# Performance work log

Hardware: AMD Instinct MI355X
Metric: run time of the kernel (lower is better)

Reference implementation:

```python
import math
import jax, jax.numpy as jnp
import numpy as np

B, T, C, H = 1, 512, 768, 12
D = C // H           # head_dim = 64
TOPK_GATE = 128      # config.hoa_top_k
EPS = 1e-5


def _ln(x, w, b):
    m = x.mean(-1, keepdims=True)
    v = ((x - m) ** 2).mean(-1, keepdims=True)
    return (x - m) * jax.lax.rsqrt(v + EPS) * w + b


def _split_heads(x):  # (B,T,C) -> (B,H,T,D)
    return x.reshape(B, T, H, D).transpose(0, 2, 1, 3)


def _sdpa_causal(q, k, v):  # (B,H,T,D) each
    s = jnp.einsum('bhtd,bhsd->bhts', q, k) / math.sqrt(D)
    t = jnp.arange(T)
    s = jnp.where(t[:, None] >= t[None, :], s, -jnp.inf)
    return jnp.einsum('bhts,bhsd->bhtd', jax.nn.softmax(s, axis=-1), v)


def _gather_time(t4, idx):
    # t4: (B,H,T,D), idx: (B,H,T,k) -> (B,H,T,k,D)
    k = idx.shape[-1]
    src = jnp.broadcast_to(t4[:, :, :, None, :], (B, H, T, k, D))
    ind = jnp.broadcast_to(idx[..., None], (B, H, T, k, D))
    return jnp.take_along_axis(src, ind, axis=2)


def _hoa(x, wq, wk1, wk2, wv1, wv2, wo):
    # order-3 higher-order attention with per-branch top-k gathered keys/values
    k_keep = max(1, math.ceil(T ** (2.0 / 3.0)))  # 64 for T=512
    scale = D ** -0.5
    q = _split_heads(x @ wq)
    tar = jnp.arange(T)
    causal_ok = tar[:, None] >= tar[None, :]          # allowed positions
    j = jnp.arange(k_keep)
    # torch code pads short rows (t+1 < k_keep) by repeating the last valid topk idx
    clip = jnp.minimum(j[None, :], tar[:, None])      # (T, k_keep)
    gK, gV = [], []
    for wk, wv in ((wk1, wv1), (wk2, wv2)):
        K = _split_heads(x @ wk)
        V = _split_heads(x @ wv)
        logits = jnp.einsum('bhtd,bhsd->bhts', q, K) * scale
        logits = jnp.where(causal_ok[None, None], logits, -jnp.inf)
        idx = jax.lax.top_k(logits, k_keep)[1]        # (B,H,T,k_keep)
        idx = jnp.take_along_axis(idx, jnp.broadcast_to(clip, idx.shape), axis=-1)
        gK.append(_gather_time(K, idx))
        gV.append(_gather_time(V, idx))
    A = jnp.einsum('bhid,bhijd,bhikd->bhijk', q, gK[0], gK[1]) * scale
    alpha = jax.nn.softmax(A, axis=-1)                # softmax over LAST axis only (as torch)
    out = jnp.einsum('bhijk,bhijd,bhikd->bhid', alpha, gV[0], gV[1])
    return out.transpose(0, 2, 1, 3).reshape(B, T, C) @ wo


def _forward(x, ln1_w, ln1_b, qkv_w, qkv_b, atto_w, atto_b,
             lnh_w, lnh_b, hq_w, hk1_w, hk2_w, hv1_w, hv2_w, ho_w,
             gate_w, gate_b, ln2_w, ln2_b, fc_w, fc_b, pr_w, pr_b):
    # causal self-attention branch
    h = _ln(x, ln1_w, ln1_b)
    qkv = h @ qkv_w + qkv_b
    q, k, v = jnp.split(qkv, 3, axis=-1)
    y = _sdpa_causal(_split_heads(q), _split_heads(k), _split_heads(v))
    y = y.transpose(0, 2, 1, 3).reshape(B, T, C) @ atto_w + atto_b
    x = x + y
    # higher-order attention branch with gated top-k token mask
    hoa_in = _ln(x, lnh_w, lnh_b)
    hoa_out = _hoa(hoa_in, hq_w, hk1_w, hk2_w, hv1_w, hv2_w, ho_w)
    scores = (hoa_in @ gate_w + gate_b)[..., 0]       # (B,T)
    kk = min(TOPK_GATE, T)
    idx = jax.lax.top_k(scores, kk)[1]                # (B,kk)
    mask = jnp.zeros((B, T), x.dtype).at[jnp.arange(B)[:, None], idx].set(1.0)
    x = x + hoa_out * mask[..., None]
    # MLP
    h2 = _ln(x, ln2_w, ln2_b)
    x = x + (jax.nn.gelu(h2 @ fc_w + fc_b, approximate=False) @ pr_w + pr_b)
    return x


def setup_inputs() -> dict:
    key = jax.random.key(0)
    ks = jax.random.split(key, 13)
    def w(k, shape):
        return jax.random.normal(k, shape, jnp.float32) * 0.02
    return dict(
        x=jax.random.normal(ks[0], (B, T, C), jnp.float32),
        ln1_w=jnp.ones(C, jnp.float32), ln1_b=jnp.zeros(C, jnp.float32),
        qkv_w=w(ks[1], (C, 3 * C)), qkv_b=jnp.zeros(3 * C, jnp.float32),
        atto_w=w(ks[2], (C, C)), atto_b=jnp.zeros(C, jnp.float32),
        lnh_w=jnp.ones(C, jnp.float32), lnh_b=jnp.zeros(C, jnp.float32),
        hq_w=w(ks[3], (C, C)), hk1_w=w(ks[4], (C, C)), hk2_w=w(ks[5], (C, C)),
        hv1_w=w(ks[6], (C, C)), hv2_w=w(ks[7], (C, C)), ho_w=w(ks[8], (C, C)),
        gate_w=w(ks[9], (C, 1)), gate_b=jnp.zeros(1, jnp.float32),
        ln2_w=jnp.ones(C, jnp.float32), ln2_b=jnp.zeros(C, jnp.float32),
        fc_w=w(ks[10], (C, 4 * C)), fc_b=jnp.zeros(4 * C, jnp.float32),
        pr_w=w(ks[11], (4 * C, C)), pr_b=jnp.zeros(C, jnp.float32),
    )


def reference(x, ln1_w, ln1_b, qkv_w, qkv_b, atto_w, atto_b,
              lnh_w, lnh_b, hq_w, hk1_w, hk2_w, hv1_w, hv2_w, ho_w,
              gate_w, gate_b, ln2_w, ln2_b, fc_w, fc_b, pr_w, pr_b):
    return _forward(x, ln1_w, ln1_b, qkv_w, qkv_b, atto_w, atto_b,
                    lnh_w, lnh_b, hq_w, hk1_w, hk2_w, hv1_w, hv2_w, ho_w,
                    gate_w, gate_b, ln2_w, ln2_b, fc_w, fc_b, pr_w, pr_b)
```

## Files before the change

### kernel.cpp

```cpp
#include <hip/hip_runtime.h>
#include <hip/hip_bf16.h>
#include <math.h>

#define TT 512
#define CC 768
#define HH 12
#define DD 64
#define KKEEP 64
#define TOPG 128
#define NTCE (TT * CC)
#define NPAIR 36
#define PW (5 * CC)

typedef __attribute__((ext_vector_type(8))) short bf16x8;
typedef __attribute__((ext_vector_type(8))) unsigned short ushort8v;
typedef __attribute__((ext_vector_type(4))) float f32x4;
typedef unsigned long long u64;

__device__ __forceinline__ float block_sum(float v, float* red) {
#pragma unroll
  for (int off = 32; off; off >>= 1) v += __shfl_xor(v, off);
  __syncthreads();
  if ((threadIdx.x & 63) == 0) red[threadIdx.x >> 6] = v;
  __syncthreads();
  return red[0] + red[1] + red[2] + red[3];
}

__device__ __forceinline__ unsigned short f32_to_bf16_rne(float f) {
  unsigned u = __float_as_uint(f);
  unsigned r = (u + 0x7FFFu + ((u >> 16) & 1u)) >> 16;
  return (unsigned short)r;
}
__device__ __forceinline__ float bf16_to_f32(unsigned short h) {
  return __uint_as_float(((unsigned)h) << 16);
}
__device__ __forceinline__ void split2(float x, unsigned short& h, unsigned short& l) {
  h = f32_to_bf16_rne(x);
  l = f32_to_bf16_rne(x - bf16_to_f32(h));
}
__device__ __forceinline__ int swz(int row, int k) {
  return row * 64 + ((((k >> 3) ^ (row & 7))) << 3) + (k & 7);
}

struct WSplitArgs {
  const float* src[10];
  unsigned short* hi[10];
  unsigned short* lo[10];
  int K[10], N[10], tstart[10];
};

__global__ __launch_bounds__(256) void wsplitT_kernel(WSplitArgs a) {
  __shared__ float tile_[64][65];
  int t = blockIdx.x;
  int wsel = 0;
#pragma unroll
  for (int i = 1; i < 10; i++)
    if (t >= a.tstart[i]) wsel = i;
  int local = t - a.tstart[wsel];
  int K = a.K[wsel], N = a.N[wsel];
  int ntn = N >> 6;
  int bn = local % ntn, bk = local / ntn;
  int tid = threadIdx.x, r = tid >> 2, cq = tid & 3;
  const float* src = a.src[wsel] + (size_t)(bk * 64 + r) * N + bn * 64 + cq * 16;
#pragma unroll
  for (int f = 0; f < 4; f++) {
    float4 v = *(const float4*)(src + f * 4);
    tile_[r][cq * 16 + f * 4 + 0] = v.x;
    tile_[r][cq * 16 + f * 4 + 1] = v.y;
    tile_[r][cq * 16 + f * 4 + 2] = v.z;
    tile_[r][cq * 16 + f * 4 + 3] = v.w;
  }
  __syncthreads();
  size_t dst = (size_t)(bn * 64 + r) * K + bk * 64 + cq * 16;
  unsigned short hv[16], lv[16];
#pragma unroll
  for (int i = 0; i < 16; i++) split2(tile_[cq * 16 + i][r], hv[i], lv[i]);
  *(ushort8v*)&a.hi[wsel][dst] = *(const ushort8v*)&hv[0];
  *(ushort8v*)&a.hi[wsel][dst + 8] = *(const ushort8v*)&hv[8];
  *(ushort8v*)&a.lo[wsel][dst] = *(const ushort8v*)&lv[0];
  *(ushort8v*)&a.lo[wsel][dst + 8] = *(const ushort8v*)&lv[8];
}

__global__ void ln_bf_kernel(const float* __restrict__ x, const float* __restrict__ w,
                             const float* __restrict__ b,
                             unsigned short* __restrict__ ohi, unsigned short* __restrict__ olo,
                             const float* __restrict__ gw, const float* __restrict__ gb,
                             float* __restrict__ gscore) {
  int t = blockIdx.x, tid = threadIdx.x;
  __shared__ float red[4];
  float ls = 0.f;
  for (int c = tid; c < CC; c += 256) ls += x[t * CC + c];
  float mean = block_sum(ls, red) * (1.f / CC);
  float lv = 0.f;
  for (int c = tid; c < CC; c += 256) { float d = x[t * CC + c] - mean; lv += d * d; }
  float var = block_sum(lv, red) * (1.f / CC);
  float rs = rsqrtf(var + 1e-5f);
  float gpart = 0.f;
  for (int c = tid; c < CC; c += 256) {
    float val = (x[t * CC + c] - mean) * rs * w[c] + b[c];
    if (gscore) gpart += val * gw[c];
    unsigned short hb, lb;
    split2(val, hb, lb);
    ohi[t * CC + c] = hb;
    olo[t * CC + c] = lb;
  }
  if (gscore) {
    float s = block_sum(gpart, red);
    if (tid == 0) gscore[t] = s + gb[0];
  }
}

__global__ __launch_bounds__(256) void gemm_bf(
    const unsigned short* __restrict__ Ah, const unsigned short* __restrict__ Al,
    const unsigned short* __restrict__ Bh, const unsigned short* __restrict__ Bl,
    const float* __restrict__ bias, float* __restrict__ Cf,
    unsigned short* __restrict__ Chi, unsigned short* __restrict__ Clo,
    int M, int N, int K, int act, int seg, const float* __restrict__ res,
    const float* __restrict__ rowmask, float* __restrict__ part) {
  __shared__ unsigned short AsH[64 * 64], AsL[64 * 64], BsH[64 * 64], BsL[64 * 64];
  int tid = threadIdx.x, lane = tid & 63, wave = tid >> 6;
  int wr = wave >> 1, wc = wave & 1, lr = lane & 15;
  int ksub = (lane >> 4) * 8;
  int n0 = blockIdx.x * 64, m0 = blockIdx.y * 64;
  int lrow = tid >> 2, lq = tid & 3;
  int kchunk = K / gridDim.z;
  int kstart = blockIdx.z * kchunk;

  f32x4 acc[2][2];
#pragma unroll
  for (int i = 0; i < 2; i++)
#pragma unroll
    for (int j = 0; j < 2; j++) acc[i][j] = (f32x4){0.f, 0.f, 0.f, 0.f};

  for (int k0 = kstart; k0 < kstart + kchunk; k0 += 64) {
    size_t aoff = (size_t)(m0 + lrow) * K + k0 + lq * 16;
    size_t boff = (size_t)(n0 + lrow) * K + k0 + lq * 16;
    int d0 = lrow * 64 + (((lq * 2) ^ (lrow & 7)) << 3);
    int d1 = lrow * 64 + (((lq * 2 + 1) ^ (lrow & 7)) << 3);
    *(ushort8v*)&AsH[d0] = *(const ushort8v*)&Ah[aoff];
    *(ushort8v*)&AsH[d1] = *(const ushort8v*)&Ah[aoff + 8];
    *(ushort8v*)&AsL[d0] = *(const ushort8v*)&Al[aoff];
    *(ushort8v*)&AsL[d1] = *(const ushort8v*)&Al[aoff + 8];
    *(ushort8v*)&BsH[d0] = *(const ushort8v*)&Bh[boff];
    *(ushort8v*)&BsH[d1] = *(const ushort8v*)&Bh[boff + 8];
    *(ushort8v*)&BsL[d0] = *(const ushort8v*)&Bl[boff];
    *(ushort8v*)&BsL[d1] = *(const ushort8v*)&Bl[boff + 8];
    __syncthreads();
#pragma unroll
    for (int kb = 0; kb < 2; kb++) {
      int kloc = kb * 32 + ksub;
      bf16x8 ah[2], al[2], bh[2], bl[2];
#pragma unroll
      for (int i = 0; i < 2; i++) {
        int m = wr * 32 + i * 16 + lr;
        int off = swz(m, kloc);
        ah[i] = *(const bf16x8*)&AsH[off];
        al[i] = *(const bf16x8*)&AsL[off];
      }
#pragma unroll
      for (int j = 0; j < 2; j++) {
        int n = wc * 32 + j * 16 + lr;
        int off = swz(n, kloc);
        bh[j] = *(const bf16x8*)&BsH[off];
        bl[j] = *(const bf16x8*)&BsL[off];
      }
#pragma unroll
      for (int i = 0; i < 2; i++)
#pragma unroll
        for (int j = 0; j < 2; j++) {
          acc[i][j] = __builtin_amdgcn_mfma_f32_16x16x32_bf16(ah[i], bh[j], acc[i][j], 0, 0, 0);
          acc[i][j] = __builtin_amdgcn_mfma_f32_16x16x32_bf16(ah[i], bl[j], acc[i][j], 0, 0, 0);
          acc[i][j] = __builtin_amdgcn_mfma_f32_16x16x32_bf16(al[i], bh[j], acc[i][j], 0, 0, 0);
        }
    }
    __syncthreads();
  }
  if (part) {
    float* pb = part + (size_t)blockIdx.z * M * N;
#pragma unroll
    for (int i = 0; i < 2; i++)
#pragma unroll
      for (int j = 0; j < 2; j++) {
        int col = n0 + wc * 32 + j * 16 + lr;
#pragma unroll
        for (int q = 0; q < 4; q++) {
          int row = m0 + wr * 32 + i * 16 + (lane >> 4) * 4 + q;
          pb[(size_t)row * N + col] = acc[i][j][q];
        }
      }
    return;
  }
#pragma unroll
  for (int i = 0; i < 2; i++)
#pragma unroll
    for (int j = 0; j < 2; j++) {
      int col = n0 + wc * 32 + j * 16 + lr;
      float bv = bias ? bias[col] : 0.f;
#pragma unroll
      for (int q = 0; q < 4; q++) {
        int row = m0 + wr * 32 + i * 16 + (lane >> 4) * 4 + q;
        float v = acc[i][j][q] + bv;
        if (act == 1) v = 0.5f * v * (1.f + erff(v * 0.70710678118654752f));
        if (rowmask) v *= rowmask[row];
        if (Cf) {
          size_t off = seg ? (size_t)(col / CC) * NTCE + (size_t)row * CC + (col % CC)
                           : (size_t)row * N + col;
          if (res) v += res[off];
          Cf[off] = v;
        }
        if (Chi) {
          size_t o2 = (size_t)row * N + col;
          unsigned short hb, lb;
          split2(v, hb, lb);
          Chi[o2] = hb;
          Clo[o2] = lb;
        }
      }
    }
}

__global__ __launch_bounds__(256) void gemm_combine_kernel(
    const float* __restrict__ part, int ksplit, int M, int N,
    const float* __restrict__ bias, float* __restrict__ Cf,
    unsigned short* __restrict__ Chi, unsigned short* __restrict__ Clo,
    int act, const float* __restrict__ res, const float* __restrict__ rowmask) {
  int i = blockIdx.x * 256 + threadIdx.x;
  if (i >= M * N) return;
  int row = i / N, col = i - row * N;
  float v = 0.f;
  for (int s = 0; s < ksplit; s++) v += part[(size_t)s * M * N + i];
  if (bias) v += bias[col];
  if (act == 1) v = 0.5f * v * (1.f + erff(v * 0.70710678118654752f));
  if (rowmask) v *= rowmask[row];
  if (Cf) {
    if (res) v += res[i];
    Cf[i] = v;
  }
  if (Chi) {
    unsigned short hb, lb;
    split2(v, hb, lb);
    Chi[i] = hb;
    Clo[i] = lb;
  }
}

__global__ __launch_bounds__(256) void sdpa_part_kernel(
    const unsigned short* __restrict__ qkvh, const unsigned short* __restrict__ qkvl,
    float* __restrict__ oPart, float* __restrict__ mPart, float* __restrict__ lPart) {
  int h = blockIdx.x;
  int p = blockIdx.y;
  int bt = 0, base = 0;
  while (p >= base + bt + 1) { base += bt + 1; bt++; }
  int st = p - base;
  int t0 = bt * 64, s0 = st * 64;
  int tid = threadIdx.x, lane = tid & 63, w = tid >> 6;
  int lr = lane & 15, ksub = (lane >> 4) * 8;
  const int hDD = h * DD;

  __shared__ unsigned short qHi[64 * 64], qLo[64 * 64];
  __shared__ unsigned short kHi[64 * 64], kLo[64 * 64];
  __shared__ unsigned short bufP[64 * 64], bufV[64 * 64];

  int lrow = tid >> 2, lq = tid & 3;
  {
    size_t qoff = (size_t)(t0 + lrow) * (3 * CC) + hDD + lq * 16;
    size_t koff = (size_t)(s0 + lrow) * (3 * CC) + CC + hDD + lq * 16;
    int d0 = lrow * 64 + (((lq * 2) ^ (lrow & 7)) << 3);
    int d1 = lrow * 64 + (((lq * 2 + 1) ^ (lrow & 7)) << 3);
    *(ushort8v*)&qHi[d0] = *(const ushort8v*)&qkvh[qoff];
    *(ushort8v*)&qHi[d1] = *(const ushort8v*)&qkvh[qoff + 8];
    *(ushort8v*)&qLo[d0] = *(const ushort8v*)&qkvl[qoff];
    *(ushort8v*)&qLo[d1] = *(const ushort8v*)&qkvl[qoff + 8];
    *(ushort8v*)&kHi[d0] = *(const ushort8v*)&qkvh[koff];
    *(ushort8v*)&kHi[d1] = *(const ushort8v*)&qkvh[koff + 8];
    *(ushort8v*)&kLo[d0] = *(const ushort8v*)&qkvl[koff];
    *(ushort8v*)&kLo[d1] = *(const ushort8v*)&qkvl[koff + 8];
  }
#pragma unroll
  for (int r = 0; r < 16; r++) {
    int sl = w * 16 + ((r + (lane >> 3)) & 15);
    bufV[swz(lane, sl)] = qkvh[(size_t)(s0 + sl) * (3 * CC) + 2 * CC + hDD + lane];
  }
  __syncthreads();
  f32x4 acc[4];
#pragma unroll
  for (int nt = 0; nt < 4; nt++) acc[nt] = (f32x4){0.f, 0.f, 0.f, 0.f};
  {
    bf16x8 ah[2], al[2];
#pragma unroll
    for (int kb = 0; kb < 2; kb++) {
      int off = swz(w * 16 + lr, kb * 32 + ksub);
      ah[kb] = *(const bf16x8*)&qHi[off];
      al[kb] = *(const bf16x8*)&qLo[off];
    }
#pragma unroll
    for (int nt = 0; nt < 4; nt++)
#pragma unroll
      for (int kb = 0; kb < 2; kb++) {
        int off = swz(nt * 16 + lr, kb * 32 + ksub);
        bf16x8 bh = *(const bf16x8*)&kHi[off];
        bf16x8 bl = *(const bf16x8*)&kLo[off];
        acc[nt] = __builtin_amdgcn_mfma_f32_16x16x32_bf16(ah[kb], bh, acc[nt], 0, 0, 0);
        acc[nt] = __builtin_amdgcn_mfma_f32_16x16x32_bf16(ah[kb], bl, acc[nt], 0, 0, 0);
        acc[nt] = __builtin_amdgcn_mfma_f32_16x16x32_bf16(al[kb], bh, acc[nt], 0, 0, 0);
      }
  }
  int pbase = (h * NPAIR + p) * 64;
#pragma unroll
  for (int q = 0; q < 4; q++) {
    int rloc = w * 16 + (lane >> 4) * 4 + q;
    float tm = -INFINITY;
#pragma unroll
    for (int nt = 0; nt < 4; nt++) {
      float v = acc[nt][q] * 0.125f;
      if (st == bt && nt * 16 + lr > rloc) v = -INFINITY;
      acc[nt][q] = v;
      tm = fmaxf(tm, v);
    }
#pragma unroll
    for (int off = 1; off < 16; off <<= 1) tm = fmaxf(tm, __shfl_xor(tm, off));
    float ps = 0.f;
#pragma unroll
    for (int nt = 0; nt < 4; nt++) {
      float e = __expf(acc[nt][q] - tm);
      acc[nt][q] = e;
      ps += e;
    }
#pragma unroll
    for (int off = 1; off < 16; off <<= 1) ps += __shfl_xor(ps, off);
    if (lr == 0) {
      mPart[pbase + rloc] = tm;
      lPart[pbase + rloc] = ps;
    }
  }
#pragma unroll
  for (int nt = 0; nt < 4; nt++)
#pragma unroll
    for (int q = 0; q < 4; q++) {
      int row = w * 16 + (lane >> 4) * 4 + q;
      int col = nt * 16 + lr;
      bufP[swz(row, col)] = f32_to_bf16_rne(acc[nt][q]);
    }
  __syncthreads();
  f32x4 o[4];
#pragma unroll
  for (int nt = 0; nt < 4; nt++) o[nt] = (f32x4){0.f, 0.f, 0.f, 0.f};
  {
    bf16x8 pf[2];
#pragma unroll
    for (int kb = 0; kb < 2; kb++)
      pf[kb] = *(const bf16x8*)&bufP[swz(w * 16 + lr, kb * 32 + ksub)];
#pragma unroll
    for (int nt = 0; nt < 4; nt++)
#pragma unroll
      for (int kb = 0; kb < 2; kb++) {
        bf16x8 bv = *(const bf16x8*)&bufV[swz(nt * 16 + lr, kb * 32 + ksub)];
        o[nt] = __builtin_amdgcn_mfma_f32_16x16x32_bf16(pf[kb], bv, o[nt], 0, 0, 0);
      }
  }
  float* obase = oPart + ((size_t)(h * NPAIR + p) << 12);
#pragma unroll
  for (int nt = 0; nt < 4; nt++)
#pragma unroll
    for (int q = 0; q < 4; q++) {
      int row = w * 16 + (lane >> 4) * 4 + q;
      int col = nt * 16 + lr;
      obase[row * 64 + col] = o[nt][q];
    }
}

__global__ __launch_bounds__(256) void sdpa_combine_kernel(
    const float* __restrict__ oPart, const float* __restrict__ mPart,
    const float* __restrict__ lPart,
    unsigned short* __restrict__ yhi, unsigned short* __restrict__ ylo) {
  int h = blockIdx.x, bt = blockIdx.y;
  int base = bt * (bt + 1) / 2;
  int n = bt + 1;
  int tid = threadIdx.x;
  int d = tid & 63;
  int r = blockIdx.z * 4 + (tid >> 6);
  int t0 = bt * 64;
  float mg = -INFINITY;
  for (int s = 0; s < n; s++)
    mg = fmaxf(mg, mPart[(h * NPAIR + base + s) * 64 + r]);
  float lg = 0.f, oacc = 0.f;
  for (int s = 0; s < n; s++) {
    int pi = h * NPAIR + base + s;
    float sc = __expf(mPart[pi * 64 + r] - mg);
    lg += sc * lPart[pi * 64 + r];
    oacc += sc * oPart[((size_t)pi << 12) + r * 64 + d];
  }
  float v = oacc / lg;
  unsigned short hb, lb;
  split2(v, hb, lb);
  yhi[(size_t)(t0 + r) * CC + h * DD + d] = hb;
  ylo[(size_t)(t0 + r) * CC + h * DD + d] = lb;
}

__global__ __launch_bounds__(256) void score_gemm_kernel(
    const unsigned short* __restrict__ ph, const unsigned short* __restrict__ pl,
    float* __restrict__ scores) {
  if (blockIdx.x > blockIdx.y) return;
  int bh = blockIdx.z;
  int br = bh >= HH ? 1 : 0;
  int h = bh - br * HH;
  int s0 = blockIdx.x * 64, t0 = blockIdx.y * 64;
  int hDD = h * DD;
  int kcol = (1 + br) * CC + hDD;
  __shared__ unsigned short AsH[64 * 64], AsL[64 * 64], BsH[64 * 64], BsL[64 * 64];
  int tid = threadIdx.x, lane = tid & 63, wave = tid >> 6;
  int wr = wave >> 1, wc = wave & 1, lr = lane & 15;
  int ksub = (lane >> 4) * 8;
  int lrow = tid >> 2, lq = tid & 3;
  {
    size_t aoff = (size_t)(t0 + lrow) * PW + hDD + lq * 16;
    size_t boff = (size_t)(s0 + lrow) * PW + kcol + lq * 16;
    int d0 = lrow * 64 + (((lq * 2) ^ (lrow & 7)) << 3);
    int d1 = lrow * 64 + (((lq * 2 + 1) ^ (lrow & 7)) << 3);
    *(ushort8v*)&AsH[d0] = *(const ushort8v*)&ph[aoff];
    *(ushort8v*)&AsH[d1] = *(const ushort8v*)&ph[aoff + 8];
    *(ushort8v*)&AsL[d0] = *(const ushort8v*)&pl[aoff];
    *(ushort8v*)&AsL[d1] = *(const ushort8v*)&pl[aoff + 8];
    *(ushort8v*)&BsH[d0] = *(const ushort8v*)&ph[boff];
    *(ushort8v*)&BsH[d1] = *(const ushort8v*)&ph[boff + 8];
    *(ushort8v*)&BsL[d0] = *(const ushort8v*)&pl[boff];
    *(ushort8v*)&BsL[d1] = *(const ushort8v*)&pl[boff + 8];
  }
  __syncthreads();
  f32x4 acc[2][2];
#pragma unroll
  for (int i = 0; i < 2; i++)
#pragma unroll
    for (int j = 0; j < 2; j++) acc[i][j] = (f32x4){0.f, 0.f, 0.f, 0.f};
#pragma unroll
  for (int kb = 0; kb < 2; kb++) {
    int kloc = kb * 32 + ksub;
    bf16x8 ah[2], al[2], bh_[2], bl[2];
#pragma unroll
    for (int i = 0; i < 2; i++) {
      int m = wr * 32 + i * 16 + lr;
      int off = swz(m, kloc);
      ah[i] = *(const bf16x8*)&AsH[off];
      al[i] = *(const bf16x8*)&AsL[off];
    }
#pragma unroll
    for (int j = 0; j < 2; j++) {
      int n = wc * 32 + j * 16 + lr;
      int off = swz(n, kloc);
      bh_[j] = *(const bf16x8*)&BsH[off];
      bl[j] = *(const bf16x8*)&BsL[off];
    }
#pragma unroll
    for (int i = 0; i < 2; i++)
#pragma unroll
      for (int j = 0; j < 2; j++) {
        acc[i][j] = __builtin_amdgcn_mfma_f32_16x16x32_bf16(ah[i], bh_[j], acc[i][j], 0, 0, 0);
        acc[i][j] = __builtin_amdgcn_mfma_f32_16x16x32_bf16(ah[i], bl[j], acc[i][j], 0, 0, 0);
        acc[i][j] = __builtin_amdgcn_mfma_f32_16x16x32_bf16(al[i], bh_[j], acc[i][j], 0, 0, 0);
      }
  }
#pragma unroll
  for (int i = 0; i < 2; i++)
#pragma unroll
    for (int j = 0; j < 2; j++)
#pragma unroll
      for (int q = 0; q < 4; q++) {
        int tt = t0 + wr * 32 + i * 16 + (lane >> 4) * 4 + q;
        int ss = s0 + wc * 32 + j * 16 + lr;
        scores[((size_t)bh * TT + tt) * TT + ss] = acc[i][j][q];
      }
}

template<int CTRL>
__device__ __forceinline__ u64 dpp64(u64 x) {
  unsigned lo = (unsigned)__builtin_amdgcn_update_dpp(
      (int)(unsigned)x, (int)(unsigned)x, CTRL, 0xF, 0xF, true);
  unsigned hi = (unsigned)__builtin_amdgcn_update_dpp(
      (int)(unsigned)(x >> 32), (int)(unsigned)(x >> 32), CTRL, 0xF, 0xF, true);
  return ((u64)hi << 32) | lo;
}
template<int MASK>
__device__ __forceinline__ u64 swz64(u64 x) {
  unsigned lo = (unsigned)__builtin_amdgcn_ds_swizzle((int)(unsigned)x, (MASK << 10) | 0x1F);
  unsigned hi = (unsigned)__builtin_amdgcn_ds_swizzle((int)(unsigned)(x >> 32), (MASK << 10) | 0x1F);
  return ((u64)hi << 32) | lo;
}
__device__ __forceinline__ u64 cas_dir(u64 x, u64 y, bool low) {
  bool take_y = low ? (y > x) : (y < x);
  return take_y ? y : x;
}
__device__ __forceinline__ u64 sort64m(u64 x, int lane) {
  x = cas_dir(x, dpp64<0xB1>(x), (lane & 1) == 0);
  x = cas_dir(x, dpp64<0x1B>(x), (lane & 2) == 0);
  x = cas_dir(x, dpp64<0xB1>(x), (lane & 1) == 0);
  x = cas_dir(x, dpp64<0x141>(x), (lane & 4) == 0);
  x = cas_dir(x, dpp64<0x4E>(x), (lane & 2) == 0);
  x = cas_dir(x, dpp64<0xB1>(x), (lane & 1) == 0);
  x = cas_dir(x, dpp64<0x140>(x), (lane & 8) == 0);
  x = cas_dir(x, swz64<4>(x), (lane & 4) == 0);
  x = cas_dir(x, dpp64<0x4E>(x), (lane & 2) == 0);
  x = cas_dir(x, dpp64<0xB1>(x), (lane & 1) == 0);
  x = cas_dir(x, swz64<31>(x), (lane & 16) == 0);
  x = cas_dir(x, swz64<8>(x), (lane & 8) == 0);
  x = cas_dir(x, swz64<4>(x), (lane & 4) == 0);
  x = cas_dir(x, dpp64<0x4E>(x), (lane & 2) == 0);
  x = cas_dir(x, dpp64<0xB1>(x), (lane & 1) == 0);
  x = cas_dir(x, __shfl_xor(x, 63), (lane & 32) == 0);
  x = cas_dir(x, swz64<16>(x), (lane & 16) == 0);
  x = cas_dir(x, swz64<8>(x), (lane & 8) == 0);
  x = cas_dir(x, swz64<4>(x), (lane & 4) == 0);
  x = cas_dir(x, dpp64<0x4E>(x), (lane & 2) == 0);
  x = cas_dir(x, dpp64<0xB1>(x), (lane & 1) == 0);
  return x;
}
__device__ __forceinline__ u64 merge64m(u64 x, int lane) {
  x = cas_dir(x, __shfl_xor(x, 32), (lane & 32) == 0);
  x = cas_dir(x, swz64<16>(x), (lane & 16) == 0);
  x = cas_dir(x, swz64<8>(x), (lane & 8) == 0);
  x = cas_dir(x, swz64<4>(x), (lane & 4) == 0);
  x = cas_dir(x, dpp64<0x4E>(x), (lane & 2) == 0);
  x = cas_dir(x, dpp64<0xB1>(x), (lane & 1) == 0);
  return x;
}
__device__ __forceinline__ u64 merge2m(u64 a, u64 b, int lane) {
  u64 rev = __shfl_xor(b, 63);
  u64 run = a > rev ? a : rev;
  return merge64m(run, lane);
}
__device__ __forceinline__ u64 make_key(float v, int s, int t) {
  unsigned sv = 0u;
  if (s <= t) {
    unsigned u = __float_as_uint(v);
    sv = (u & 0x80000000u) ? ~u : (u | 0x80000000u);
  }
  return ((u64)sv << 32) | (unsigned)(~s);
}

__global__ __launch_bounds__(256) void topk_select_kernel(
    const float* __restrict__ scores, int* __restrict__ idx1, int* __restrict__ idx2) {
  int tid = threadIdx.x, lane = tid & 63, w = tid >> 6;
  int row = blockIdx.x * 4 + w;
  int br = row >= (HH * TT) ? 1 : 0;
  int rem = row - br * (HH * TT);
  int h = rem >> 9, t = rem & (TT - 1);
  const float* sr = scores + ((size_t)(br * HH + h) * TT + t) * TT;
  int nc = (t >> 6) + 1;
  u64 c[8];
#pragma unroll
  for (int e = 0; e < 8; e++) {
    if (e < nc)
      c[e] = sort64m(make_key(sr[e * 64 + lane], e * 64 + lane, t), lane);
    else
      c[e] = (u64)(unsigned)(~(e * 64 + lane));
  }
  u64 l10 = (t >= 64)  ? merge2m(c[0], c[1], lane) : c[0];
  u64 l11 = (t >= 192) ? merge2m(c[2], c[3], lane) : c[2];
  u64 l12 = (t >= 320) ? merge2m(c[4], c[5], lane) : c[4];
  u64 l13 = (t >= 448) ? merge2m(c[6], c[7], lane) : c[6];
  u64 l20 = (t >= 128) ? merge2m(l10, l11, lane) : l10;
  u64 l21 = (t >= 384) ? merge2m(l12, l13, lane) : l12;
  u64 res = (t >= 256) ? merge2m(l20, l21, lane) : l20;
  unsigned myidx = ~(unsigned)res;
  unsigned outv = __shfl(myidx, min(lane, t));
  int* idxout = (br ? idx2 : idx1) + ((size_t)h * TT + t) * KKEEP;
  idxout[lane] = (int)outv;
}

__device__ __forceinline__ u64 cas_u64(u64 x, int j, bool dirmax, int lane) {
  u64 y = __shfl_xor(x, j);
  bool lower = (lane & j) == 0;
  bool keepmax = (dirmax == lower);
  return (keepmax ? (y > x) : (y < x)) ? y : x;
}
__device__ __forceinline__ void sort512(u64* key, int lane) {
#pragma unroll
  for (int k = 2; k <= 512; k <<= 1) {
#pragma unroll
    for (int j = k >> 1; j > 0; j >>= 1) {
      if (j < 64) {
        bool lower = (lane & j) == 0;
#pragma unroll
        for (int e = 0; e < 8; e++) {
          bool desc = ((((e << 6) | lane) & k) == 0);
          u64 part = __shfl_xor(key[e], j);
          bool wantmax = (desc == lower);
          key[e] = (wantmax ? (part > key[e]) : (part < key[e])) ? part : key[e];
        }
      } else {
        int m = j >> 6;
#pragma unroll
        for (int e = 0; e < 8; e++) {
          if ((e & m) == 0) {
            int e2 = e | m;
            bool desc = ((((e << 6) | lane) & k) == 0);
            u64 a = key[e], b = key[e2];
            u64 mx = a > b ? a : b;
            u64 mn = a > b ? b : a;
            key[e] = desc ? mx : mn;
            key[e2] = desc ? mn : mx;
          }
        }
      }
    }
  }
}

__global__ __launch_bounds__(256) void hoa_core_kernel(
    const unsigned short* __restrict__ ph, const unsigned short* __restrict__ pl,
    const int* __restrict__ idx1, const int* __restrict__ idx2,
    unsigned short* __restrict__ hcohi, unsigned short* __restrict__ hcolo) {
  int h = blockIdx.x, t = blockIdx.y, tid = threadIdx.x;
  int lane = tid & 63, w = tid >> 6;
  int lr = lane & 15;
  int ksub = (lane >> 4) * 8;
  const int hDD = h * DD;

  __shared__ unsigned short bufA[64 * 64];
  __shared__ unsigned short bufB[64 * 64];
  __shared__ unsigned short v1s[64 * 68];
  __shared__ float red[4 * 64];
  __shared__ int i1s[64], i2s[64];

  if (tid < 64) {
    i1s[tid] = idx1[(h * TT + t) * KKEEP + tid] * PW + CC + hDD;
    i2s[tid] = idx2[(h * TT + t) * KKEEP + tid] * PW + 2 * CC + hDD;
  }
  __syncthreads();

  size_t qoff = (size_t)t * PW + hDD + lane;
  float qreg = bf16_to_f32(ph[qoff]) + bf16_to_f32(pl[qoff]);

#pragma unroll
  for (int r = 0; r < 16; r++) {
    int j = w * 16 + r;
    float k1v = bf16_to_f32(ph[i1s[j] + lane]);
    int off = swz(j, lane);
    bufA[off] = f32_to_bf16_rne(k1v * qreg);
    bufB[off] = ph[i2s[j] + lane];
    v1s[j * 68 + lane] = ph[i1s[j] + 2 * CC + lane];
  }
  __syncthreads();

  f32x4 acc[4];
#pragma unroll
  for (int nt = 0; nt < 4; nt++) acc[nt] = (f32x4){0.f, 0.f, 0.f, 0.f};
  {
    bf16x8 af[2];
#pragma unroll
    for (int kb = 0; kb < 2; kb++)
      af[kb] = *(const bf16x8*)&bufA[swz(w * 16 + lr, kb * 32 + ksub)];
#pragma unroll
    for (int nt = 0; nt < 4; nt++)
#pragma unroll
      for (int kb = 0; kb < 2; kb++) {
        bf16x8 bf = *(const bf16x8*)&bufB[swz(nt * 16 + lr, kb * 32 + ksub)];
        acc[nt] = __builtin_amdgcn_mfma_f32_16x16x32_bf16(af[kb], bf, acc[nt], 0, 0, 0);
      }
  }
#pragma unroll
  for (int q = 0; q < 4; q++) {
    float m = -INFINITY;
#pragma unroll
    for (int nt = 0; nt < 4; nt++) {
      acc[nt][q] *= 0.125f;
      m = fmaxf(m, acc[nt][q]);
    }
#pragma unroll
    for (int off = 1; off < 16; off <<= 1) m = fmaxf(m, __shfl_xor(m, off));
    float s = 0.f;
#pragma unroll
    for (int nt = 0; nt < 4; nt++) {
      float e = __expf(acc[nt][q] - m);
      acc[nt][q] = e;
      s += e;
    }
#pragma unroll
    for (int off = 1; off < 16; off <<= 1) s += __shfl_xor(s, off);
    float inv = 1.f / s;
#pragma unroll
    for (int nt = 0; nt < 4; nt++) acc[nt][q] *= inv;
  }
  __syncthreads();

#pragma unroll
  for (int nt = 0; nt < 4; nt++)
#pragma unroll
    for (int q = 0; q < 4; q++) {
      int row = w * 16 + (lane >> 4) * 4 + q;
      int col = nt * 16 + lr;
      bufA[swz(row, col)] = f32_to_bf16_rne(acc[nt][q]);
    }
#pragma unroll
  for (int r = 0; r < 16; r++) {
    int kk = w * 16 + ((r + (lane >> 3)) & 15);
    bufB[swz(lane, kk)] = ph[i2s[kk] + 2 * CC + lane];
  }
  __syncthreads();

  f32x4 acc2[4];
#pragma unroll
  for (int nt = 0; nt < 4; nt++) acc2[nt] = (f32x4){0.f, 0.f, 0.f, 0.f};
  {
    bf16x8 af[2];
#pragma unroll
    for (int kb = 0; kb < 2; kb++)
      af[kb] = *(const bf16x8*)&bufA[swz(w * 16 + lr, kb * 32 + ksub)];
#pragma unroll
    for (int nt = 0; nt < 4; nt++)
#pragma unroll
      for (int kb = 0; kb < 2; kb++) {
        bf16x8 bf = *(const bf16x8*)&bufB[swz(nt * 16 + lr, kb * 32 + ksub)];
        acc2[nt] = __builtin_amdgcn_mfma_f32_16x16x32_bf16(af[kb], bf, acc2[nt], 0, 0, 0);
      }
  }
#pragma unroll
  for (int nt = 0; nt < 4; nt++) {
    float p = 0.f;
#pragma unroll
    for (int q = 0; q < 4; q++) {
      int row = w * 16 + (lane >> 4) * 4 + q;
      int col = lr + 16 * nt;
      p += acc2[nt][q] * bf16_to_f32(v1s[row * 68 + col]);
    }
    p += __shfl_xor(p, 16);
    p += __shfl_xor(p, 32);
    if (lane < 16) red[w * 64 + 16 * nt + lr] = p;
  }
  __syncthreads();
  if (tid < 64) {
    float o = red[tid] + red[64 + tid] + red[128 + tid] + red[192 + tid];
    unsigned short hb, lb;
    split2(o, hb, lb);
    hcohi[t * CC + hDD + tid] = hb;
    hcolo[t * CC + hDD + tid] = lb;
  }
}

__global__ void gate_mask_kernel(const float* __restrict__ scores, float* __restrict__ mask) {
  int lane = threadIdx.x;
  u64 key[8];
#pragma unroll
  for (int e = 0; e < 8; e++) {
    int s = e * 64 + lane;
    unsigned uu = __float_as_uint(scores[s]);
    unsigned sv = (uu & 0x80000000u) ? ~uu : (uu | 0x80000000u);
    key[e] = ((u64)sv << 32) | (unsigned)(~s);
    mask[s] = 0.f;
  }
  __asm__ volatile("s_waitcnt vmcnt(0)" ::: "memory");
  sort512(key, lane);
#pragma unroll
  for (int e = 0; e < 2; e++) mask[(int)(~(unsigned)key[e])] = 1.f;
}

extern "C" void kernel_launch(void* const* d_in, const int* in_sizes, int n_in,
                              void* d_out, int out_size, void* d_ws, size_t ws_size,
                              hipStream_t stream) {
  const float* x      = (const float*)d_in[0];
  const float* ln1_w  = (const float*)d_in[1];
  const float* ln1_b  = (const float*)d_in[2];
  const float* qkv_w  = (const float*)d_in[3];
  const float* qkv_b  = (const float*)d_in[4];
  const float* atto_w = (const float*)d_in[5];
  const float* atto_b = (const float*)d_in[6];
  const float* lnh_w  = (const float*)d_in[7];
  const float* lnh_b  = (const float*)d_in[8];
  const float* hq_w   = (const float*)d_in[9];
  const float* hk1_w  = (const float*)d_in[10];
  const float* hk2_w  = (const float*)d_in[11];
  const float* hv1_w  = (const float*)d_in[12];
  const float* hv2_w  = (const float*)d_in[13];
  const float* ho_w   = (const float*)d_in[14];
  const float* gate_w = (const float*)d_in[15];
  const float* gate_b = (const float*)d_in[16];
  const float* ln2_w  = (const float*)d_in[17];
  const float* ln2_b  = (const float*)d_in[18];
  const float* fc_w   = (const float*)d_in[19];
  const float* fc_b   = (const float*)d_in[20];
  const float* pr_w   = (const float*)d_in[21];
  const float* pr_b   = (const float*)d_in[22];
  float* out = (float*)d_out;

  char* cur = (char*)d_ws;
  auto alloc = [&](size_t bytes) {
    char* p = cur;
    cur += (bytes + 255) & ~(size_t)255;
    return p;
  };
  float* x1   = (float*)alloc((size_t)NTCE * 4);
  float* x2   = (float*)alloc((size_t)NTCE * 4);
  float* scores = (float*)alloc(TT * 4);
  float* maskb  = (float*)alloc(TT * 4);
  int* idx1 = (int*)alloc((size_t)HH * TT * KKEEP * 4);
  int* idx2 = (int*)alloc((size_t)HH * TT * KKEEP * 4);
  float* hscores = (float*)alloc((size_t)2 * HH * TT * TT * 4);
  float* oPart = (float*)alloc((size_t)HH * NPAIR * 64 * 64 * 4);
  float* mPart = (float*)alloc((size_t)HH * NPAIR * 64 * 4);
  float* lPart = (float*)alloc((size_t)HH * NPAIR * 64 * 4);
  float* gpart = (float*)alloc((size_t)2 * TT * 4 * CC * 4);
  unsigned short* hHi    = (unsigned short*)alloc((size_t)NTCE * 2);
  unsigned short* hLo    = (unsigned short*)alloc((size_t)NTCE * 2);
  unsigned short* qkvHi  = (unsigned short*)alloc((size_t)3 * NTCE * 2);
  unsigned short* qkvLo  = (unsigned short*)alloc((size_t)3 * NTCE * 2);
  unsigned short* yHi    = (unsigned short*)alloc((size_t)NTCE * 2);
  unsigned short* yLo    = (unsigned short*)alloc((size_t)NTCE * 2);
  unsigned short* hoinHi = (unsigned short*)alloc((size_t)NTCE * 2);
  unsigned short* hoinLo = (unsigned short*)alloc((size_t)NTCE * 2);
  unsigned short* hoaPh  = (unsigned short*)alloc((size_t)TT * PW * 2);
  unsigned short* hoaPl  = (unsigned short*)alloc((size_t)TT * PW * 2);
  unsigned short* h2Hi   = (unsigned short*)alloc((size_t)NTCE * 2);
  unsigned short* h2Lo   = (unsigned short*)alloc((size_t)NTCE * 2);
  unsigned short* hcoHi  = (unsigned short*)alloc((size_t)NTCE * 2);
  unsigned short* hcoLo  = (unsigned short*)alloc((size_t)NTCE * 2);
  unsigned short* fcbHi  = (unsigned short*)alloc((size_t)4 * NTCE * 2);
  unsigned short* fcbLo  = (unsigned short*)alloc((size_t)4 * NTCE * 2);
  const size_t WSQ = (size_t)CC * CC;
  unsigned short* qkvT_h = (unsigned short*)alloc((size_t)CC * 3 * CC * 2);
  unsigned short* qkvT_l = (unsigned short*)alloc((size_t)CC * 3 * CC * 2);
  unsigned short* attoT_h = (unsigned short*)alloc(WSQ * 2);
  unsigned short* attoT_l = (unsigned short*)alloc(WSQ * 2);
  unsigned short* hoaT_h = (unsigned short*)alloc(5 * WSQ * 2);
  unsigned short* hoaT_l = (unsigned short*)alloc(5 * WSQ * 2);
  unsigned short* hoT_h = (unsigned short*)alloc(WSQ * 2);
  unsigned short* hoT_l = (unsigned short*)alloc(WSQ * 2);
  unsigned short* fcT_h = (unsigned short*)alloc((size_t)CC * 4 * CC * 2);
  unsigned short* fcT_l = (unsigned short*)alloc((size_t)CC * 4 * CC * 2);
  unsigned short* prT_h = (unsigned short*)alloc((size_t)CC * 4 * CC * 2);
  unsigned short* prT_l = (unsigned short*)alloc((size_t)CC * 4 * CC * 2);

  WSplitArgs wa;
  int tcur = 0;
  auto addw = [&](int i, const float* s, unsigned short* hi, unsigned short* lo, int K, int N) {
    wa.src[i] = s; wa.hi[i] = hi; wa.lo[i] = lo;
    wa.K[i] = K; wa.N[i] = N; wa.tstart[i] = tcur;
    tcur += (N / 64) * (K / 64);
  };
  addw(0, qkv_w, qkvT_h, qkvT_l, CC, 3 * CC);
  addw(1, atto_w, attoT_h, attoT_l, CC, CC);
  addw(2, hq_w,  hoaT_h + 0 * WSQ, hoaT_l + 0 * WSQ, CC, CC);
  addw(3, hk1_w, hoaT_h + 1 * WSQ, hoaT_l + 1 * WSQ, CC, CC);
  addw(4, hk2_w, hoaT_h + 2 * WSQ, hoaT_l + 2 * WSQ, CC, CC);
  addw(5, hv1_w, hoaT_h + 3 * WSQ, hoaT_l + 3 * WSQ, CC, CC);
  addw(6, hv2_w, hoaT_h + 4 * WSQ, hoaT_l + 4 * WSQ, CC, CC);
  addw(7, ho_w, hoT_h, hoT_l, CC, CC);
  addw(8, fc_w, fcT_h, fcT_l, CC, 4 * CC);
  addw(9, pr_w, prT_h, prT_l, 4 * CC, CC);

  dim3 blk(256);
  const float* nullf = nullptr;

  hipLaunchKernelGGL(wsplitT_kernel, dim3(tcur), blk, 0, stream, wa);
  hipLaunchKernelGGL(ln_bf_kernel, dim3(TT), blk, 0, stream, x, ln1_w, ln1_b,
                     hHi, hLo, nullf, nullf, (float*)nullptr);
  hipLaunchKernelGGL(gemm_bf, dim3(36, 8, 2), blk, 0, stream, hHi, hLo, qkvT_h, qkvT_l,
                     nullf, (float*)nullptr, (unsigned short*)nullptr, (unsigned short*)nullptr,
                     TT, 3 * CC, CC, 0, 0, nullf, nullf, gpart);
  hipLaunchKernelGGL(gemm_combine_kernel, dim3((TT * 3 * CC + 255) / 256), blk, 0, stream,
                     gpart, 2, TT, 3 * CC, qkv_b, (float*)nullptr,
                     qkvHi, qkvLo, 0, nullf, nullf);
  hipLaunchKernelGGL(sdpa_part_kernel, dim3(HH, NPAIR), blk, 0, stream,
                     qkvHi, qkvLo, oPart, mPart, lPart);
  hipLaunchKernelGGL(sdpa_combine_kernel, dim3(HH, 8, 16), blk, 0, stream,
                     oPart, mPart, lPart, yHi, yLo);
  hipLaunchKernelGGL(gemm_bf, dim3(12, 8, 2), blk, 0, stream, yHi, yLo, attoT_h, attoT_l,
                     nullf, (float*)nullptr, (unsigned short*)nullptr, (unsigned short*)nullptr,
                     TT, CC, CC, 0, 0, nullf, nullf, gpart);
  hipLaunchKernelGGL(gemm_combine_kernel, dim3((NTCE + 255) / 256), blk, 0, stream,
                     gpart, 2, TT, CC, atto_b, x1,
                     (unsigned short*)nullptr, (unsigned short*)nullptr, 0, x, nullf);
  hipLaunchKernelGGL(ln_bf_kernel, dim3(TT), blk, 0, stream, x1, lnh_w, lnh_b,
                     hoinHi, hoinLo, gate_w, gate_b, scores);
  hipLaunchKernelGGL(gate_mask_kernel, dim3(1), dim3(64), 0, stream, scores, maskb);
  hipLaunchKernelGGL(gemm_bf, dim3(60, 8, 1), blk, 0, stream, hoinHi, hoinLo, hoaT_h, hoaT_l,
                     nullf, (float*)nullptr, hoaPh, hoaPl,
                     TT, PW, CC, 0, 0, nullf, nullf, (float*)nullptr);
  hipLaunchKernelGGL(score_gemm_kernel, dim3(8, 8, 2 * HH), blk, 0, stream,
                     hoaPh, hoaPl, hscores);
  hipLaunchKernelGGL(topk_select_kernel, dim3(2 * HH * TT / 4), blk, 0, stream,
                     hscores, idx1, idx2);
  hipLaunchKernelGGL(hoa_core_kernel, dim3(HH, TT), blk, 0, stream,
                     hoaPh, hoaPl, idx1, idx2, hcoHi, hcoLo);
  hipLaunchKernelGGL(gemm_bf, dim3(12, 8, 2), blk, 0, stream, hcoHi, hcoLo, hoT_h, hoT_l,
                     nullf, (float*)nullptr, (unsigned short*)nullptr, (unsigned short*)nullptr,
                     TT, CC, CC, 0, 0, nullf, nullf, gpart);
  hipLaunchKernelGGL(gemm_combine_kernel, dim3((NTCE + 255) / 256), blk, 0, stream,
                     gpart, 2, TT, CC, nullf, x2,
                     (unsigned short*)nullptr, (unsigned short*)nullptr, 0, x1, maskb);
  hipLaunchKernelGGL(ln_bf_kernel, dim3(TT), blk, 0, stream, x2, ln2_w, ln2_b,
                     h2Hi, h2Lo, nullf, nullf, (float*)nullptr);
  hipLaunchKernelGGL(gemm_bf, dim3(48, 8, 2), blk, 0, stream, h2Hi, h2Lo, fcT_h, fcT_l,
                     nullf, (float*)nullptr, (unsigned short*)nullptr, (unsigned short*)nullptr,
                     TT, 4 * CC, CC, 1, 0, nullf, nullf, gpart);
  hipLaunchKernelGGL(gemm_combine_kernel, dim3((TT * 4 * CC + 255) / 256), blk, 0, stream,
                     gpart, 2, TT, 4 * CC, fc_b, (float*)nullptr,
                     fcbHi, fcbLo, 1, nullf, nullf);
  hipLaunchKernelGGL(gemm_bf, dim3(12, 8, 4), blk, 0, stream, fcbHi, fcbLo, prT_h, prT_l,
                     nullf, (float*)nullptr, (unsigned short*)nullptr, (unsigned short*)nullptr,
                     TT, CC, 4 * CC, 0, 0, nullf, nullf, gpart);
  hipLaunchKernelGGL(gemm_combine_kernel, dim3((NTCE + 255) / 256), blk, 0, stream,
                     gpart, 4, TT, CC, pr_b, out,
                     (unsigned short*)nullptr, (unsigned short*)nullptr, 0, x2, nullf);
}
```

Measured before the change: 251.7 us.

## Drop split-K for QKV and FC GEMMs and pack hoa_core gathers into 32-bit accesses

The QKV and FC GEMMs now run without split-K. Each writes its biased (and for FC, activated) bf16 hi/lo outputs directly, so the two gemm_combine launches and the fp32 partial round-trip go away. In hoa_core_kernel, the gathered K1/K2/V1 loads and their LDS stores now move two bf16 values per 32-bit access, and the transposed V2 fill packs two rows per store. In exchange the two GEMMs launch half as many blocks, with a longer K loop per block, which can lower occupancy and parallelism.

```diff
diff --git a/kernel.cpp b/kernel.cpp
--- a/kernel.cpp
+++ b/kernel.cpp
@@ -627,17 +627,23 @@
   }
   __syncthreads();
 
-  size_t qoff = (size_t)t * PW + hDD + lane;
-  float qreg = bf16_to_f32(ph[qoff]) + bf16_to_f32(pl[qoff]);
-
-#pragma unroll
-  for (int r = 0; r < 16; r++) {
-    int j = w * 16 + r;
-    float k1v = bf16_to_f32(ph[i1s[j] + lane]);
-    int off = swz(j, lane);
-    bufA[off] = f32_to_bf16_rne(k1v * qreg);
-    bufB[off] = ph[i2s[j] + lane];
-    v1s[j * 68 + lane] = ph[i1s[j] + 2 * CC + lane];
+  int half = lane >> 5;
+  int c2 = (lane & 31) * 2;
+  size_t qbase = (size_t)t * PW + hDD;
+  float qf0 = bf16_to_f32(ph[qbase + c2]) + bf16_to_f32(pl[qbase + c2]);
+  float qf1 = bf16_to_f32(ph[qbase + c2 + 1]) + bf16_to_f32(pl[qbase + c2 + 1]);
+#pragma unroll
+  for (int r = 0; r < 8; r++) {
+    int j = w * 16 + r * 2 + half;
+    unsigned k1p = *(const unsigned*)&ph[i1s[j] + c2];
+    unsigned k2p = *(const unsigned*)&ph[i2s[j] + c2];
+    unsigned v1p = *(const unsigned*)&ph[i1s[j] + 2 * CC + c2];
+    unsigned short a0 = f32_to_bf16_rne(bf16_to_f32((unsigned short)(k1p & 0xFFFFu)) * qf0);
+    unsigned short a1 = f32_to_bf16_rne(bf16_to_f32((unsigned short)(k1p >> 16)) * qf1);
+    int off = swz(j, c2);
+    *(unsigned*)&bufA[off] = (unsigned)a0 | ((unsigned)a1 << 16);
+    *(unsigned*)&bufB[off] = k2p;
+    *(unsigned*)&v1s[j * 68 + c2] = v1p;
   }
   __syncthreads();
 
@@ -691,9 +697,12 @@
       bufA[swz(row, col)] = f32_to_bf16_rne(acc[nt][q]);
     }
 #pragma unroll
-  for (int r = 0; r < 16; r++) {
-    int kk = w * 16 + ((r + (lane >> 3)) & 15);
-    bufB[swz(lane, kk)] = ph[i2s[kk] + 2 * CC + lane];
+  for (int r = 0; r < 8; r++) {
+    int kk = w * 16 + ((r * 2 + ((lane >> 3) * 2)) & 15);
+    unsigned short b0 = ph[i2s[kk] + 2 * CC + lane];
+    unsigned short b1 = ph[i2s[kk + 1] + 2 * CC + lane];
+    int off = swz(lane, kk);
+    *(unsigned*)&bufB[off] = (unsigned)b0 | ((unsigned)b1 << 16);
   }
   __syncthreads();
 
@@ -852,12 +861,9 @@
   hipLaunchKernelGGL(wsplitT_kernel, dim3(tcur), blk, 0, stream, wa);
   hipLaunchKernelGGL(ln_bf_kernel, dim3(TT), blk, 0, stream, x, ln1_w, ln1_b,
                      hHi, hLo, nullf, nullf, (float*)nullptr);
-  hipLaunchKernelGGL(gemm_bf, dim3(36, 8, 2), blk, 0, stream, hHi, hLo, qkvT_h, qkvT_l,
-                     nullf, (float*)nullptr, (unsigned short*)nullptr, (unsigned short*)nullptr,
-                     TT, 3 * CC, CC, 0, 0, nullf, nullf, gpart);
-  hipLaunchKernelGGL(gemm_combine_kernel, dim3((TT * 3 * CC + 255) / 256), blk, 0, stream,
-                     gpart, 2, TT, 3 * CC, qkv_b, (float*)nullptr,
-                     qkvHi, qkvLo, 0, nullf, nullf);
+  hipLaunchKernelGGL(gemm_bf, dim3(36, 8, 1), blk, 0, stream, hHi, hLo, qkvT_h, qkvT_l,
+                     qkv_b, (float*)nullptr, qkvHi, qkvLo,
+                     TT, 3 * CC, CC, 0, 0, nullf, nullf, (float*)nullptr);
   hipLaunchKernelGGL(sdpa_part_kernel, dim3(HH, NPAIR), blk, 0, stream,
                      qkvHi, qkvLo, oPart, mPart, lPart);
   hipLaunchKernelGGL(sdpa_combine_kernel, dim3(HH, 8, 16), blk, 0, stream,
@@ -888,12 +894,9 @@
                      (unsigned short*)nullptr, (unsigned short*)nullptr, 0, x1, maskb);
   hipLaunchKernelGGL(ln_bf_kernel, dim3(TT), blk, 0, stream, x2, ln2_w, ln2_b,
                      h2Hi, h2Lo, nullf, nullf, (float*)nullptr);
-  hipLaunchKernelGGL(gemm_bf, dim3(48, 8, 2), blk, 0, stream, h2Hi, h2Lo, fcT_h, fcT_l,
-                     nullf, (float*)nullptr, (unsigned short*)nullptr, (unsigned short*)nullptr,
-                     TT, 4 * CC, CC, 1, 0, nullf, nullf, gpart);
-  hipLaunchKernelGGL(gemm_combine_kernel, dim3((TT * 4 * CC + 255) / 256), blk, 0, stream,
-                     gpart, 2, TT, 4 * CC, fc_b, (float*)nullptr,
-                     fcbHi, fcbLo, 1, nullf, nullf);
+  hipLaunchKernelGGL(gemm_bf, dim3(48, 8, 1), blk, 0, stream, h2Hi, h2Lo, fcT_h, fcT_l,
+                     fc_b, (float*)nullptr, fcbHi, fcbLo,
+                     TT, 4 * CC, CC, 1, 0, nullf, nullf, (float*)nullptr);
   hipLaunchKernelGGL(gemm_bf, dim3(12, 8, 4), blk, 0, stream, fcbHi, fcbLo, prT_h, prT_l,
                      nullf, (float*)nullptr, (unsigned short*)nullptr, (unsigned short*)nullptr,
                      TT, CC, 4 * CC, 0, 0, nullf, nullf, gpart);
```

Measured after the change: 249.7 us. Within noise of the previous version (-0.8%).
